# Optimization experiments

Hardware: AMD Instinct MI355X
Metric: run time of the kernel (lower is better)

## Reference

```python
import jax, jax.numpy as jnp
import numpy as np

NUM_WIRES = 14
LAYERS = 3
PPL = 3
BATCH = 1024
DIM = 2 ** NUM_WIRES


def setup_inputs() -> dict:
    key = jax.random.key(0)
    k1, k2, k3, k4, k5 = jax.random.split(key, 5)
    sr = jax.random.normal(k1, (BATCH, DIM), jnp.float32)
    si = jax.random.normal(k2, (BATCH, DIM), jnp.float32)
    norm = jnp.sqrt(jnp.sum(sr * sr + si * si, axis=1, keepdims=True))
    sr, si = sr / norm, si / norm  # normalized amplitude-encoded states
    weights = jax.random.normal(k3, (LAYERS, PPL, NUM_WIRES), jnp.float32)
    head_w = jax.random.normal(k4, (1, NUM_WIRES), jnp.float32) / np.sqrt(NUM_WIRES)
    head_b = jax.random.normal(k5, (1,), jnp.float32) * 0.01
    return {"state_real": sr, "state_imag": si, "weights": weights,
            "head_w": head_w, "head_b": head_b}


def _apply_ry_all(st, angles):
    # st: (B,)+(2,)*n complex; apply RY(angles[q]) on each wire q (RYs on distinct wires commute)
    half = angles * 0.5
    c, s = jnp.cos(half), jnp.sin(half)
    for q in range(NUM_WIRES):
        ax = 1 + q
        a0 = jnp.take(st, 0, axis=ax)
        a1 = jnp.take(st, 1, axis=ax)
        n0 = c[q] * a0 - s[q] * a1
        n1 = s[q] * a0 + c[q] * a1
        st = jnp.stack([n0, n1], axis=ax)
    return st


def _apply_cnot(st, ctrl, tgt):
    # flip target axis only where control bit == 1
    ctrl_ax, tgt_ax = 1 + ctrl, 1 + tgt
    flipped = jnp.flip(st, axis=tgt_ax)
    mask_shape = [1] * (NUM_WIRES + 1)
    mask_shape[ctrl_ax] = 2
    mask = (jnp.arange(2).reshape(mask_shape) == 1)
    return jnp.where(mask, flipped, st)


def _circuit(state, weights):
    # state: (B, DIM) complex64 -> PauliZ expvals (B, NUM_WIRES)
    st = state.reshape((-1,) + (2,) * NUM_WIRES)
    for l in range(LAYERS):
        # sequential RY(w[l,p,q]) for p=0..PPL-1 on wire q compose to RY(sum_p w[l,p,q])
        ang = jnp.sum(weights[l], axis=0)  # (NUM_WIRES,)
        st = _apply_ry_all(st, ang)
        for j in range(NUM_WIRES):
            st = _apply_cnot(st, j, (j + 1) % NUM_WIRES)
    probs = st.real ** 2 + st.imag ** 2  # (B,)+(2,)*n
    probs = probs.reshape(-1, DIM)
    idx = jnp.arange(DIM)
    # PennyLane convention: wire 0 is the most significant bit
    bits = (idx[None, :] >> (NUM_WIRES - 1 - jnp.arange(NUM_WIRES))[:, None]) & 1  # (n, DIM)
    signs = (1 - 2 * bits).astype(probs.dtype)
    return probs @ signs.T  # (B, n)


def reference(state_real, state_imag, weights, head_w, head_b):
    state = jax.lax.complex(state_real, state_imag)
    feats = _circuit(state, weights)  # (B, NUM_WIRES)
    return feats @ head_w[0] + head_b[0]  # (B,)
```

## Files before the change

kernel.cpp:

```cpp
#include <hip/hip_runtime.h>

typedef unsigned int u32;

#define DIM 16384
#define NT  512

__host__ __device__ constexpr u32 swzN(u32 d) {
    u32 b0 = ((d >> 4) ^ (d >> 5)) & 1u;
    u32 b1 = (d >> 4) & 1u;
    u32 b2 = ((d >> 7) ^ (d >> 8)) & 1u;
    u32 b3 = ((d >> 6) ^ (d >> 8)) & 1u;
    return d ^ b0 ^ (b1 << 1) ^ (b2 << 2) ^ (b3 << 3);
}

__host__ __device__ constexpr u32 mmap(u32 y) {
    u32 s = y;
    s ^= s >> 1; s ^= s >> 2; s ^= s >> 4; s ^= s >> 8;
    return (s & 0x1FFFu) | (((s ^ (y >> 13)) & 1u) << 13);
}

__host__ __device__ constexpr u32 mpow(u32 x, int L) {
    for (int i = 0; i < L; ++i) x = mmap(x);
    return x;
}

constexpr u32 PV3[5] = {0x040, 0x080, 0x100, 0x200, 0x400};
constexpr u32 PV4[5] = {0x006, 0x00C, 0x018, 0x030, 0x060};
constexpr u32 PV5[5] = {0x3001, 0x0003, 0x0C00, 0x1800, 0x3000};
constexpr u32 PV6[5] = {0x005, 0x00A, 0x014, 0x028, 0x050};
constexpr u32 PV7[5] = {0x0A0, 0x140, 0x280, 0x500, 0xA00};

__host__ __device__ constexpr u32 moff(const u32* v, int r) {
    u32 m = 0;
    for (int i = 0; i < 5; ++i) if ((r >> i) & 1) m ^= v[i];
    return m;
}
__host__ __device__ constexpr u32 parmask(const u32* v, int L, int b) {
    u32 pm = 0;
    for (int r = 0; r < 32; ++r)
        pm |= ((mpow(moff(v, r), L) >> b) & 1u) << r;
    return pm;
}
__host__ __device__ constexpr int hbit(int D) {
    int h = 0;
    while (D >> (h + 1)) ++h;
    return 1 << h;
}

__device__ __forceinline__ void rot2(float2& a0, float2& a1, float c, float s) {
    float t0x = s * a1.x, t0y = s * a1.y;
    float t1x = s * a0.x, t1y = s * a0.y;
    float n0x = fmaf(c, a0.x, -t0x), n0y = fmaf(c, a0.y, -t0y);
    float n1x = fmaf(c, a1.x,  t1x), n1y = fmaf(c, a1.y,  t1y);
    a0.x = n0x; a0.y = n0y;
    a1.x = n1x; a1.y = n1y;
}

template<int D, u32 PM>
__device__ __forceinline__ void gateGM(float2 (&am)[32], float c, float s, u32 sB) {
    constexpr int H = hbit(D);
    float sp = sB ? -s : s;
    #pragma unroll
    for (int r = 0; r < 32; ++r)
        if (!(r & H)) {
            if ((PM >> r) & 1) rot2(am[r], am[r ^ D], c, -sp);
            else               rot2(am[r], am[r ^ D], c,  sp);
        }
}

__global__ __launch_bounds__(NT, 2) void qsim_kernel(
    const float* __restrict__ sreal, const float* __restrict__ simag,
    const float* __restrict__ wts,   const float* __restrict__ hw,
    const float* __restrict__ hb,    float* __restrict__ out)
{
    extern __shared__ float smem[];
    float* angC   = smem + 32768;
    float* angS   = angC + 48;
    float* lutLo  = angS + 48;
    float* lutHi  = lutLo + 128;
    float* redbuf = lutHi + 128;
    float2* st2 = (float2*)smem;
    float4* stv = (float4*)smem;

    int tid = threadIdx.x;
    int b   = blockIdx.x;

    const float4* pr = (const float4*)(sreal + (size_t)b * DIM);
    const float4* pi = (const float4*)(simag + (size_t)b * DIM);
    float4 vr[8], vi[8];
    #pragma unroll
    for (int h = 0; h < 8; ++h) {
        vr[h] = pr[(h << 9) | tid];
        vi[h] = pi[(h << 9) | tid];
    }

    if (tid < 42) {
        int l = tid / 14, bb = tid % 14, q = 13 - bb;
        float a = 0.5f * (wts[l * 42 + q] + wts[l * 42 + 14 + q] + wts[l * 42 + 28 + q]);
        angC[l * 16 + bb] = cosf(a);
        angS[l * 16 + bb] = sinf(a);
    } else if (tid >= 64 && tid < 192) {
        int i = tid - 64;
        float ssum = 0.f;
        for (int bb = 0; bb < 7; ++bb) if ((i >> bb) & 1) ssum += hw[13 - bb];
        lutLo[i] = ssum;
    } else if (tid >= 192 && tid < 320) {
        int i = tid - 192;
        float ssum = 0.f;
        for (int bb = 0; bb < 7; ++bb) if ((i >> bb) & 1) ssum += hw[6 - bb];
        lutHi[i] = ssum;
    }

    float2 am[32];
    #pragma unroll
    for (int h = 0; h < 8; ++h) {
        am[h * 4 + 0] = make_float2(vr[h].x, vi[h].x);
        am[h * 4 + 1] = make_float2(vr[h].y, vi[h].y);
        am[h * 4 + 2] = make_float2(vr[h].z, vi[h].z);
        am[h * 4 + 3] = make_float2(vr[h].w, vi[h].w);
    }

    __syncthreads();
    float W0  = lutLo[127] + lutHi[127];
    float acc = 0.f;

    {
        gateGM< 1, 0>(am, angC[ 0], angS[ 0], 0);
        gateGM< 2, 0>(am, angC[ 1], angS[ 1], 0);
        gateGM< 4, 0>(am, angC[11], angS[11], 0);
        gateGM< 8, 0>(am, angC[12], angS[12], 0);
        gateGM<16, 0>(am, angC[13], angS[13], 0);
        u32 base = swzN((u32)tid << 2);
        bool sw = (((tid >> 2) ^ (tid >> 3)) & 1) != 0;
        #pragma unroll
        for (int h = 0; h < 8; ++h)
            #pragma unroll
            for (int m = 0; m < 2; ++m) {
                u32 idx = (base ^ swzN(((u32)h << 11) | ((u32)m << 1))) >> 1;
                int r = h * 4 + m * 2;
                float2 a0 = am[r], a1 = am[r + 1];
                stv[idx] = sw ? make_float4(a1.x, a1.y, a0.x, a0.y)
                              : make_float4(a0.x, a0.y, a1.x, a1.y);
            }
        __syncthreads();
    }

    {
        u32 yb = (((u32)tid & 1u) << 1) | (((u32)tid >> 1) << 6);
        u32 base = swzN(yb);
        #pragma unroll
        for (int h = 0; h < 16; ++h) {
            u32 idx = (base ^ swzN((u32)h << 2)) >> 1;
            float4 v = stv[idx];
            if (((h >> 2) ^ (h >> 3)) & 1) {
                am[h * 2 + 1] = make_float2(v.x, v.y);
                am[h * 2]     = make_float2(v.z, v.w);
            } else {
                am[h * 2]     = make_float2(v.x, v.y);
                am[h * 2 + 1] = make_float2(v.z, v.w);
            }
        }
        gateGM< 2, 0>(am, angC[2], angS[2], 0);
        gateGM< 4, 0>(am, angC[3], angS[3], 0);
        gateGM< 8, 0>(am, angC[4], angS[4], 0);
        gateGM<16, 0>(am, angC[5], angS[5], 0);
        #pragma unroll
        for (int h = 0; h < 16; ++h) {
            u32 idx = (base ^ swzN((u32)h << 2)) >> 1;
            float2 a0 = am[h * 2], a1 = am[h * 2 + 1];
            if (((h >> 2) ^ (h >> 3)) & 1) stv[idx] = make_float4(a1.x, a1.y, a0.x, a0.y);
            else                           stv[idx] = make_float4(a0.x, a0.y, a1.x, a1.y);
        }
        __syncthreads();
    }

    {
        u32 B = ((u32)tid & 63u) | (((u32)tid >> 6) << 11);
        u32 base = swzN(B);
        #pragma unroll
        for (int j = 0; j < 32; ++j) am[j] = st2[base ^ swzN((u32)j << 6)];
        gateGM< 1, 0>(am, angC[ 6], angS[ 6], 0);
        gateGM< 2, 0>(am, angC[ 7], angS[ 7], 0);
        gateGM< 4, 0>(am, angC[ 8], angS[ 8], 0);
        gateGM< 8, 0>(am, angC[ 9], angS[ 9], 0);
        gateGM<16, 0>(am, angC[10], angS[10], 0);
        u32 z1 = mmap(B);
        gateGM< 3, parmask(PV3, 1,  7)>(am, angC[16 +  7], angS[16 +  7], (z1 >>  7) & 1u);
        gateGM< 6, parmask(PV3, 1,  8)>(am, angC[16 +  8], angS[16 +  8], (z1 >>  8) & 1u);
        gateGM<12, parmask(PV3, 1,  9)>(am, angC[16 +  9], angS[16 +  9], (z1 >>  9) & 1u);
        gateGM<24, parmask(PV3, 1, 10)>(am, angC[16 + 10], angS[16 + 10], (z1 >> 10) & 1u);
        #pragma unroll
        for (int j = 0; j < 32; ++j) st2[base ^ swzN((u32)j << 6)] = am[j];
        __syncthreads();
    }

    {
        u32 B = ((u32)tid & 3u) | (((u32)tid >> 2) << 7);
        u32 base = swzN(B);
        #pragma unroll
        for (int r = 0; r < 32; ++r) am[r] = st2[base ^ swzN(moff(PV4, r))];
        u32 z1 = mmap(B);
        gateGM< 1, parmask(PV4, 1, 2)>(am, angC[16 + 2], angS[16 + 2], (z1 >> 2) & 1u);
        gateGM< 2, parmask(PV4, 1, 3)>(am, angC[16 + 3], angS[16 + 3], (z1 >> 3) & 1u);
        gateGM< 4, parmask(PV4, 1, 4)>(am, angC[16 + 4], angS[16 + 4], (z1 >> 4) & 1u);
        gateGM< 8, parmask(PV4, 1, 5)>(am, angC[16 + 5], angS[16 + 5], (z1 >> 5) & 1u);
        gateGM<16, parmask(PV4, 1, 6)>(am, angC[16 + 6], angS[16 + 6], (z1 >> 6) & 1u);
        #pragma unroll
        for (int r = 0; r < 32; ++r) st2[base ^ swzN(moff(PV4, r))] = am[r];
        __syncthreads();
    }

    {
        u32 B = (((u32)tid & 0xFFu) << 2) | (((u32)tid >> 8) << 13);
        u32 base = swzN(B);
        #pragma unroll
        for (int r = 0; r < 32; ++r) am[r] = st2[base ^ swzN(moff(PV5, r))];
        u32 z1 = mmap(B), z2 = mmap(z1);
        gateGM< 1, parmask(PV5, 1,  0)>(am, angC[16 +  0], angS[16 +  0], (z1 >>  0) & 1u);
        gateGM< 2, parmask(PV5, 1,  1)>(am, angC[16 +  1], angS[16 +  1], (z1 >>  1) & 1u);
        gateGM< 4, parmask(PV5, 1, 11)>(am, angC[16 + 11], angS[16 + 11], (z1 >> 11) & 1u);
        gateGM< 8, parmask(PV5, 1, 12)>(am, angC[16 + 12], angS[16 + 12], (z1 >> 12) & 1u);
        gateGM<16, parmask(PV5, 1, 13)>(am, angC[16 + 13], angS[16 + 13], (z1 >> 13) & 1u);
        gateGM<25, parmask(PV5, 2,  0)>(am, angC[32 +  0], angS[32 +  0], (z2 >>  0) & 1u);
        gateGM< 3, parmask(PV5, 2,  1)>(am, angC[32 +  1], angS[32 +  1], (z2 >>  1) & 1u);
        gateGM<12, parmask(PV5, 2, 12)>(am, angC[32 + 12], angS[32 + 12], (z2 >> 12) & 1u);
        gateGM<24, parmask(PV5, 2, 13)>(am, angC[32 + 13], angS[32 + 13], (z2 >> 13) & 1u);
        #pragma unroll
        for (int r = 0; r < 32; ++r) st2[base ^ swzN(moff(PV5, r))] = am[r];
        __syncthreads();
    }

    {
        u32 B = ((u32)tid & 3u) | (((u32)tid >> 2) << 7);
        u32 base = swzN(B);
        #pragma unroll
        for (int r = 0; r < 32; ++r) am[r] = st2[base ^ swzN(moff(PV6, r))];
        u32 z2 = mpow(B, 2);
        gateGM< 1, parmask(PV6, 2, 2)>(am, angC[32 + 2], angS[32 + 2], (z2 >> 2) & 1u);
        gateGM< 2, parmask(PV6, 2, 3)>(am, angC[32 + 3], angS[32 + 3], (z2 >> 3) & 1u);
        gateGM< 4, parmask(PV6, 2, 4)>(am, angC[32 + 4], angS[32 + 4], (z2 >> 4) & 1u);
        gateGM< 8, parmask(PV6, 2, 5)>(am, angC[32 + 5], angS[32 + 5], (z2 >> 5) & 1u);
        gateGM<16, parmask(PV6, 2, 6)>(am, angC[32 + 6], angS[32 + 6], (z2 >> 6) & 1u);
        #pragma unroll
        for (int r = 0; r < 32; ++r) st2[base ^ swzN(moff(PV6, r))] = am[r];
        __syncthreads();
    }

    {
        u32 B = ((u32)tid & 0x7Fu) | (((u32)tid >> 7) << 12);
        u32 base = swzN(B);
        #pragma unroll
        for (int r = 0; r < 32; ++r) am[r] = st2[base ^ swzN(moff(PV7, r))];
        u32 z2 = mpow(B, 2);
        gateGM< 1, parmask(PV7, 2,  7)>(am, angC[32 +  7], angS[32 +  7], (z2 >>  7) & 1u);
        gateGM< 2, parmask(PV7, 2,  8)>(am, angC[32 +  8], angS[32 +  8], (z2 >>  8) & 1u);
        gateGM< 4, parmask(PV7, 2,  9)>(am, angC[32 +  9], angS[32 +  9], (z2 >>  9) & 1u);
        gateGM< 8, parmask(PV7, 2, 10)>(am, angC[32 + 10], angS[32 + 10], (z2 >> 10) & 1u);
        gateGM<16, parmask(PV7, 2, 11)>(am, angC[32 + 11], angS[32 + 11], (z2 >> 11) & 1u);
        u32 wB = mmap(z2);
        #pragma unroll
        for (int r = 0; r < 32; ++r) {
            u32 w = wB ^ mpow(moff(PV7, r), 3);
            float p  = fmaf(am[r].x, am[r].x, am[r].y * am[r].y);
            float wv = W0 - 2.0f * (lutLo[w & 127u] + lutHi[w >> 7]);
            acc = fmaf(wv, p, acc);
        }
    }

    #pragma unroll
    for (int off = 32; off > 0; off >>= 1) acc += __shfl_xor(acc, off, 64);
    if ((tid & 63) == 0) redbuf[tid >> 6] = acc;
    __syncthreads();
    if (tid == 0) {
        float tot = hb[0];
        #pragma unroll
        for (int i = 0; i < 8; ++i) tot += redbuf[i];
        out[b] = tot;
    }
}

extern "C" void kernel_launch(void* const* d_in, const int* in_sizes, int n_in,
                              void* d_out, int out_size, void* d_ws, size_t ws_size,
                              hipStream_t stream)
{
    const float* sreal = (const float*)d_in[0];
    const float* simag = (const float*)d_in[1];
    const float* wts   = (const float*)d_in[2];
    const float* hw    = (const float*)d_in[3];
    const float* hb    = (const float*)d_in[4];
    float* out = (float*)d_out;

    int batch = in_sizes[0] / DIM;
    size_t smem_bytes = (32768 + 48 + 48 + 128 + 128 + 16) * sizeof(float);

    (void)hipFuncSetAttribute((const void*)qsim_kernel,
                              hipFuncAttributeMaxDynamicSharedMemorySize, (int)smem_bytes);
    qsim_kernel<<<dim3(batch), dim3(NT), smem_bytes, stream>>>(sreal, simag, wts, hw, hb, out);
}
```

Baseline: 208.9 us.

## Halve shared state buffer by exchanging in two half-block phases for occupancy

Each shared-memory transpose between gate groups is split into two rounds: half of the threads (selected by tid bit 6 or 7) write and read back their half of the state through a 64 KB buffer instead of 128 KB, using a compacted index. This halves LDS per block so launch bounds can request 4 blocks per SM instead of 2, aiming to improve latency hiding. It also drops the separate vr/vi staging registers. In exchange, each exchange now needs four barriers instead of one, and the higher occupancy target caps registers for the 32-element complex amplitude array, risking spills.

```diff
diff --git a/kernel.cpp b/kernel.cpp
--- a/kernel.cpp
+++ b/kernel.cpp
@@ -18,7 +18,6 @@
     s ^= s >> 1; s ^= s >> 2; s ^= s >> 4; s ^= s >> 8;
     return (s & 0x1FFFu) | (((s ^ (y >> 13)) & 1u) << 13);
 }
-
 __host__ __device__ constexpr u32 mpow(u32 x, int L) {
     for (int i = 0; i < L; ++i) x = mmap(x);
     return x;
@@ -45,6 +44,9 @@
     int h = 0;
     while (D >> (h + 1)) ++h;
     return 1 << h;
+}
+__host__ __device__ constexpr u32 cmpt(u32 s, int t) {
+    return (s & ((1u << t) - 1u)) | ((s >> (t + 1)) << t);
 }
 
 __device__ __forceinline__ void rot2(float2& a0, float2& a1, float c, float s) {
@@ -68,30 +70,216 @@
         }
 }
 
-__global__ __launch_bounds__(NT, 2) void qsim_kernel(
+__device__ __forceinline__ u32 B2of(int t) {
+    return ((u32)(t & 1) << 1) | ((u32)((t >> 1) & 3) << 6) | ((u32)((t >> 6) & 1) << 8)
+         | ((u32)((t >> 3) & 7) << 9) | ((u32)((t >> 7) & 3) << 12);
+}
+__device__ __forceinline__ u32 B3of(int t) { return ((u32)t & 63u) | (((u32)t >> 6) << 11); }
+__device__ __forceinline__ u32 B4of(int t) {
+    return (u32)(t & 3) | ((u32)((t >> 2) & 1) << 7) | ((u32)((t >> 6) & 1) << 8)
+         | ((u32)((t >> 3) & 7) << 9) | ((u32)((t >> 7) & 3) << 12);
+}
+__device__ __forceinline__ u32 B5of(int t) { return (((u32)t & 0xFFu) << 2) | (((u32)t >> 8) << 13); }
+__device__ __forceinline__ u32 B7of(int t) { return ((u32)t & 0x7Fu) | (((u32)t >> 7) << 12); }
+
+__device__ __forceinline__ void doG1(float2 (&am)[32], const float* angC, const float* angS) {
+    gateGM< 1, 0>(am, angC[ 0], angS[ 0], 0);
+    gateGM< 2, 0>(am, angC[ 1], angS[ 1], 0);
+    gateGM< 4, 0>(am, angC[11], angS[11], 0);
+    gateGM< 8, 0>(am, angC[12], angS[12], 0);
+    gateGM<16, 0>(am, angC[13], angS[13], 0);
+}
+__device__ __forceinline__ void doG2(float2 (&am)[32], const float* angC, const float* angS) {
+    gateGM< 2, 0>(am, angC[2], angS[2], 0);
+    gateGM< 4, 0>(am, angC[3], angS[3], 0);
+    gateGM< 8, 0>(am, angC[4], angS[4], 0);
+    gateGM<16, 0>(am, angC[5], angS[5], 0);
+}
+__device__ __forceinline__ void doG3(int tid, float2 (&am)[32], const float* angC, const float* angS) {
+    gateGM< 1, 0>(am, angC[ 6], angS[ 6], 0);
+    gateGM< 2, 0>(am, angC[ 7], angS[ 7], 0);
+    gateGM< 4, 0>(am, angC[ 8], angS[ 8], 0);
+    gateGM< 8, 0>(am, angC[ 9], angS[ 9], 0);
+    gateGM<16, 0>(am, angC[10], angS[10], 0);
+    u32 z1 = mmap(B3of(tid));
+    gateGM< 3, parmask(PV3, 1,  7)>(am, angC[16 +  7], angS[16 +  7], (z1 >>  7) & 1u);
+    gateGM< 6, parmask(PV3, 1,  8)>(am, angC[16 +  8], angS[16 +  8], (z1 >>  8) & 1u);
+    gateGM<12, parmask(PV3, 1,  9)>(am, angC[16 +  9], angS[16 +  9], (z1 >>  9) & 1u);
+    gateGM<24, parmask(PV3, 1, 10)>(am, angC[16 + 10], angS[16 + 10], (z1 >> 10) & 1u);
+}
+__device__ __forceinline__ void doG4(int tid, float2 (&am)[32], const float* angC, const float* angS) {
+    u32 z1 = mmap(B4of(tid));
+    gateGM< 1, parmask(PV4, 1, 2)>(am, angC[16 + 2], angS[16 + 2], (z1 >> 2) & 1u);
+    gateGM< 2, parmask(PV4, 1, 3)>(am, angC[16 + 3], angS[16 + 3], (z1 >> 3) & 1u);
+    gateGM< 4, parmask(PV4, 1, 4)>(am, angC[16 + 4], angS[16 + 4], (z1 >> 4) & 1u);
+    gateGM< 8, parmask(PV4, 1, 5)>(am, angC[16 + 5], angS[16 + 5], (z1 >> 5) & 1u);
+    gateGM<16, parmask(PV4, 1, 6)>(am, angC[16 + 6], angS[16 + 6], (z1 >> 6) & 1u);
+}
+__device__ __forceinline__ void doG5(int tid, float2 (&am)[32], const float* angC, const float* angS) {
+    u32 z1 = mmap(B5of(tid)), z2 = mmap(z1);
+    gateGM< 1, parmask(PV5, 1,  0)>(am, angC[16 +  0], angS[16 +  0], (z1 >>  0) & 1u);
+    gateGM< 2, parmask(PV5, 1,  1)>(am, angC[16 +  1], angS[16 +  1], (z1 >>  1) & 1u);
+    gateGM< 4, parmask(PV5, 1, 11)>(am, angC[16 + 11], angS[16 + 11], (z1 >> 11) & 1u);
+    gateGM< 8, parmask(PV5, 1, 12)>(am, angC[16 + 12], angS[16 + 12], (z1 >> 12) & 1u);
+    gateGM<16, parmask(PV5, 1, 13)>(am, angC[16 + 13], angS[16 + 13], (z1 >> 13) & 1u);
+    gateGM<25, parmask(PV5, 2,  0)>(am, angC[32 +  0], angS[32 +  0], (z2 >>  0) & 1u);
+    gateGM< 3, parmask(PV5, 2,  1)>(am, angC[32 +  1], angS[32 +  1], (z2 >>  1) & 1u);
+    gateGM<12, parmask(PV5, 2, 12)>(am, angC[32 + 12], angS[32 + 12], (z2 >> 12) & 1u);
+    gateGM<24, parmask(PV5, 2, 13)>(am, angC[32 + 13], angS[32 + 13], (z2 >> 13) & 1u);
+}
+__device__ __forceinline__ void doG6(int tid, float2 (&am)[32], const float* angC, const float* angS) {
+    u32 z2 = mpow(B4of(tid), 2);
+    gateGM< 1, parmask(PV6, 2, 2)>(am, angC[32 + 2], angS[32 + 2], (z2 >> 2) & 1u);
+    gateGM< 2, parmask(PV6, 2, 3)>(am, angC[32 + 3], angS[32 + 3], (z2 >> 3) & 1u);
+    gateGM< 4, parmask(PV6, 2, 4)>(am, angC[32 + 4], angS[32 + 4], (z2 >> 4) & 1u);
+    gateGM< 8, parmask(PV6, 2, 5)>(am, angC[32 + 5], angS[32 + 5], (z2 >> 5) & 1u);
+    gateGM<16, parmask(PV6, 2, 6)>(am, angC[32 + 6], angS[32 + 6], (z2 >> 6) & 1u);
+}
+__device__ __forceinline__ void doG7(int tid, float2 (&am)[32], const float* angC, const float* angS) {
+    u32 z2 = mpow(B7of(tid), 2);
+    gateGM< 1, parmask(PV7, 2,  7)>(am, angC[32 +  7], angS[32 +  7], (z2 >>  7) & 1u);
+    gateGM< 2, parmask(PV7, 2,  8)>(am, angC[32 +  8], angS[32 +  8], (z2 >>  8) & 1u);
+    gateGM< 4, parmask(PV7, 2,  9)>(am, angC[32 +  9], angS[32 +  9], (z2 >>  9) & 1u);
+    gateGM< 8, parmask(PV7, 2, 10)>(am, angC[32 + 10], angS[32 + 10], (z2 >> 10) & 1u);
+    gateGM<16, parmask(PV7, 2, 11)>(am, angC[32 + 11], angS[32 + 11], (z2 >> 11) & 1u);
+}
+__device__ __forceinline__ void doMeas(int tid, float2 (&am)[32], const float* lutLo,
+                                       const float* lutHi, float& acc, float W0) {
+    u32 wB = mpow(B7of(tid), 3);
+    #pragma unroll
+    for (int r = 0; r < 32; ++r) {
+        u32 w = wB ^ mpow(moff(PV7, r), 3);
+        float p  = fmaf(am[r].x, am[r].x, am[r].y * am[r].y);
+        float wv = W0 - 2.0f * (lutLo[w & 127u] + lutHi[w >> 7]);
+        acc = fmaf(wv, p, acc);
+    }
+}
+
+__device__ __forceinline__ void doW1(int tid, float* smem, float2 (&am)[32]) {
+    float4* stv = (float4*)smem;
+    u32 base = cmpt(swzN((u32)tid << 2), 8);
+    bool sw = (((tid >> 2) ^ (tid >> 3)) & 1) != 0;
+    #pragma unroll
+    for (int h = 0; h < 8; ++h)
+        #pragma unroll
+        for (int m = 0; m < 2; ++m) {
+            u32 idx = (base ^ (((u32)h << 10) | ((u32)m << 1))) >> 1;
+            int r = h * 4 + m * 2;
+            float2 a0 = am[r], a1 = am[r + 1];
+            stv[idx] = sw ? make_float4(a1.x, a1.y, a0.x, a0.y)
+                          : make_float4(a0.x, a0.y, a1.x, a1.y);
+        }
+}
+__device__ __forceinline__ void doR2(int tid, float* smem, float2 (&am)[32]) {
+    float4* stv = (float4*)smem;
+    u32 base = cmpt(swzN(B2of(tid)), 8);
+    #pragma unroll
+    for (int h = 0; h < 16; ++h) {
+        u32 idx = (base ^ swzN((u32)h << 2)) >> 1;
+        float4 v = stv[idx];
+        if (((h >> 2) ^ (h >> 3)) & 1) {
+            am[h * 2 + 1] = make_float2(v.x, v.y);
+            am[h * 2]     = make_float2(v.z, v.w);
+        } else {
+            am[h * 2]     = make_float2(v.x, v.y);
+            am[h * 2 + 1] = make_float2(v.z, v.w);
+        }
+    }
+}
+__device__ __forceinline__ void doW2(int tid, float* smem, float2 (&am)[32]) {
+    float4* stv = (float4*)smem;
+    u32 base = cmpt(swzN(B2of(tid)), 12);
+    #pragma unroll
+    for (int h = 0; h < 16; ++h) {
+        u32 idx = (base ^ swzN((u32)h << 2)) >> 1;
+        float2 a0 = am[h * 2], a1 = am[h * 2 + 1];
+        if (((h >> 2) ^ (h >> 3)) & 1) stv[idx] = make_float4(a1.x, a1.y, a0.x, a0.y);
+        else                           stv[idx] = make_float4(a0.x, a0.y, a1.x, a1.y);
+    }
+}
+__device__ __forceinline__ void doR3(int tid, float* smem, float2 (&am)[32]) {
+    float2* st2 = (float2*)smem;
+    u32 base = cmpt(swzN(B3of(tid)), 12);
+    #pragma unroll
+    for (int j = 0; j < 32; ++j) am[j] = st2[base ^ swzN((u32)j << 6)];
+}
+__device__ __forceinline__ void doW3(int tid, float* smem, float2 (&am)[32]) {
+    float2* st2 = (float2*)smem;
+    u32 base = cmpt(swzN(B3of(tid)), 12);
+    #pragma unroll
+    for (int j = 0; j < 32; ++j) st2[base ^ swzN((u32)j << 6)] = am[j];
+}
+__device__ __forceinline__ void doR4(int tid, float* smem, float2 (&am)[32]) {
+    float2* st2 = (float2*)smem;
+    u32 base = cmpt(swzN(B4of(tid)), 12);
+    #pragma unroll
+    for (int r = 0; r < 32; ++r) am[r] = st2[base ^ swzN(moff(PV4, r))];
+}
+__device__ __forceinline__ void doW4(int tid, float* smem, float2 (&am)[32]) {
+    float2* st2 = (float2*)smem;
+    u32 base = cmpt(swzN(B4of(tid)), 8);
+    #pragma unroll
+    for (int r = 0; r < 32; ++r) st2[base ^ swzN(moff(PV4, r))] = am[r];
+}
+__device__ __forceinline__ void doR5(int tid, float* smem, float2 (&am)[32]) {
+    float2* st2 = (float2*)smem;
+    u32 base = cmpt(swzN(B5of(tid)), 8);
+    #pragma unroll
+    for (int r = 0; r < 32; ++r) am[r] = st2[base ^ cmpt(moff(PV5, r), 8)];
+}
+__device__ __forceinline__ void doW5(int tid, float* smem, float2 (&am)[32]) {
+    float2* st2 = (float2*)smem;
+    u32 base = cmpt(swzN(B5of(tid)), 8);
+    #pragma unroll
+    for (int r = 0; r < 32; ++r) st2[base ^ cmpt(moff(PV5, r), 8)] = am[r];
+}
+__device__ __forceinline__ void doR6(int tid, float* smem, float2 (&am)[32]) {
+    float2* st2 = (float2*)smem;
+    u32 base = cmpt(swzN(B4of(tid)), 8);
+    #pragma unroll
+    for (int r = 0; r < 32; ++r) am[r] = st2[base ^ swzN(moff(PV6, r))];
+}
+__device__ __forceinline__ void doW6(int tid, float* smem, float2 (&am)[32]) {
+    float2* st2 = (float2*)smem;
+    u32 base = cmpt(swzN(B4of(tid)), 12);
+    #pragma unroll
+    for (int r = 0; r < 32; ++r) st2[base ^ swzN(moff(PV6, r))] = am[r];
+}
+__device__ __forceinline__ void doR7(int tid, float* smem, float2 (&am)[32]) {
+    float2* st2 = (float2*)smem;
+    u32 base = cmpt(swzN(B7of(tid)), 12);
+    #pragma unroll
+    for (int r = 0; r < 32; ++r) am[r] = st2[base ^ swzN(moff(PV7, r))];
+}
+
+__global__ __launch_bounds__(NT, 4) void qsim_kernel(
     const float* __restrict__ sreal, const float* __restrict__ simag,
     const float* __restrict__ wts,   const float* __restrict__ hw,
     const float* __restrict__ hb,    float* __restrict__ out)
 {
     extern __shared__ float smem[];
-    float* angC   = smem + 32768;
+    float* angC   = smem + 16384;
     float* angS   = angC + 48;
     float* lutLo  = angS + 48;
     float* lutHi  = lutLo + 128;
     float* redbuf = lutHi + 128;
-    float2* st2 = (float2*)smem;
-    float4* stv = (float4*)smem;
 
     int tid = threadIdx.x;
     int b   = blockIdx.x;
+    int r6  = (tid >> 6) & 1;
+    int r7  = (tid >> 7) & 1;
 
     const float4* pr = (const float4*)(sreal + (size_t)b * DIM);
     const float4* pi = (const float4*)(simag + (size_t)b * DIM);
-    float4 vr[8], vi[8];
+    float2 am[32];
     #pragma unroll
     for (int h = 0; h < 8; ++h) {
-        vr[h] = pr[(h << 9) | tid];
-        vi[h] = pi[(h << 9) | tid];
+        float4 r = pr[(h << 9) | tid];
+        float4 i = pi[(h << 9) | tid];
+        am[h * 4 + 0] = make_float2(r.x, i.x);
+        am[h * 4 + 1] = make_float2(r.y, i.y);
+        am[h * 4 + 2] = make_float2(r.z, i.z);
+        am[h * 4 + 3] = make_float2(r.w, i.w);
     }
 
     if (tid < 42) {
@@ -111,161 +299,42 @@
         lutHi[i] = ssum;
     }
 
-    float2 am[32];
-    #pragma unroll
-    for (int h = 0; h < 8; ++h) {
-        am[h * 4 + 0] = make_float2(vr[h].x, vi[h].x);
-        am[h * 4 + 1] = make_float2(vr[h].y, vi[h].y);
-        am[h * 4 + 2] = make_float2(vr[h].z, vi[h].z);
-        am[h * 4 + 3] = make_float2(vr[h].w, vi[h].w);
-    }
-
     __syncthreads();
     float W0  = lutLo[127] + lutHi[127];
     float acc = 0.f;
 
-    {
-        gateGM< 1, 0>(am, angC[ 0], angS[ 0], 0);
-        gateGM< 2, 0>(am, angC[ 1], angS[ 1], 0);
-        gateGM< 4, 0>(am, angC[11], angS[11], 0);
-        gateGM< 8, 0>(am, angC[12], angS[12], 0);
-        gateGM<16, 0>(am, angC[13], angS[13], 0);
-        u32 base = swzN((u32)tid << 2);
-        bool sw = (((tid >> 2) ^ (tid >> 3)) & 1) != 0;
-        #pragma unroll
-        for (int h = 0; h < 8; ++h)
-            #pragma unroll
-            for (int m = 0; m < 2; ++m) {
-                u32 idx = (base ^ swzN(((u32)h << 11) | ((u32)m << 1))) >> 1;
-                int r = h * 4 + m * 2;
-                float2 a0 = am[r], a1 = am[r + 1];
-                stv[idx] = sw ? make_float4(a1.x, a1.y, a0.x, a0.y)
-                              : make_float4(a0.x, a0.y, a1.x, a1.y);
-            }
-        __syncthreads();
-    }
-
-    {
-        u32 yb = (((u32)tid & 1u) << 1) | (((u32)tid >> 1) << 6);
-        u32 base = swzN(yb);
-        #pragma unroll
-        for (int h = 0; h < 16; ++h) {
-            u32 idx = (base ^ swzN((u32)h << 2)) >> 1;
-            float4 v = stv[idx];
-            if (((h >> 2) ^ (h >> 3)) & 1) {
-                am[h * 2 + 1] = make_float2(v.x, v.y);
-                am[h * 2]     = make_float2(v.z, v.w);
-            } else {
-                am[h * 2]     = make_float2(v.x, v.y);
-                am[h * 2 + 1] = make_float2(v.z, v.w);
-            }
-        }
-        gateGM< 2, 0>(am, angC[2], angS[2], 0);
-        gateGM< 4, 0>(am, angC[3], angS[3], 0);
-        gateGM< 8, 0>(am, angC[4], angS[4], 0);
-        gateGM<16, 0>(am, angC[5], angS[5], 0);
-        #pragma unroll
-        for (int h = 0; h < 16; ++h) {
-            u32 idx = (base ^ swzN((u32)h << 2)) >> 1;
-            float2 a0 = am[h * 2], a1 = am[h * 2 + 1];
-            if (((h >> 2) ^ (h >> 3)) & 1) stv[idx] = make_float4(a1.x, a1.y, a0.x, a0.y);
-            else                           stv[idx] = make_float4(a0.x, a0.y, a1.x, a1.y);
-        }
-        __syncthreads();
-    }
-
-    {
-        u32 B = ((u32)tid & 63u) | (((u32)tid >> 6) << 11);
-        u32 base = swzN(B);
-        #pragma unroll
-        for (int j = 0; j < 32; ++j) am[j] = st2[base ^ swzN((u32)j << 6)];
-        gateGM< 1, 0>(am, angC[ 6], angS[ 6], 0);
-        gateGM< 2, 0>(am, angC[ 7], angS[ 7], 0);
-        gateGM< 4, 0>(am, angC[ 8], angS[ 8], 0);
-        gateGM< 8, 0>(am, angC[ 9], angS[ 9], 0);
-        gateGM<16, 0>(am, angC[10], angS[10], 0);
-        u32 z1 = mmap(B);
-        gateGM< 3, parmask(PV3, 1,  7)>(am, angC[16 +  7], angS[16 +  7], (z1 >>  7) & 1u);
-        gateGM< 6, parmask(PV3, 1,  8)>(am, angC[16 +  8], angS[16 +  8], (z1 >>  8) & 1u);
-        gateGM<12, parmask(PV3, 1,  9)>(am, angC[16 +  9], angS[16 +  9], (z1 >>  9) & 1u);
-        gateGM<24, parmask(PV3, 1, 10)>(am, angC[16 + 10], angS[16 + 10], (z1 >> 10) & 1u);
-        #pragma unroll
-        for (int j = 0; j < 32; ++j) st2[base ^ swzN((u32)j << 6)] = am[j];
-        __syncthreads();
-    }
-
-    {
-        u32 B = ((u32)tid & 3u) | (((u32)tid >> 2) << 7);
-        u32 base = swzN(B);
-        #pragma unroll
-        for (int r = 0; r < 32; ++r) am[r] = st2[base ^ swzN(moff(PV4, r))];
-        u32 z1 = mmap(B);
-        gateGM< 1, parmask(PV4, 1, 2)>(am, angC[16 + 2], angS[16 + 2], (z1 >> 2) & 1u);
-        gateGM< 2, parmask(PV4, 1, 3)>(am, angC[16 + 3], angS[16 + 3], (z1 >> 3) & 1u);
-        gateGM< 4, parmask(PV4, 1, 4)>(am, angC[16 + 4], angS[16 + 4], (z1 >> 4) & 1u);
-        gateGM< 8, parmask(PV4, 1, 5)>(am, angC[16 + 5], angS[16 + 5], (z1 >> 5) & 1u);
-        gateGM<16, parmask(PV4, 1, 6)>(am, angC[16 + 6], angS[16 + 6], (z1 >> 6) & 1u);
-        #pragma unroll
-        for (int r = 0; r < 32; ++r) st2[base ^ swzN(moff(PV4, r))] = am[r];
-        __syncthreads();
-    }
-
-    {
-        u32 B = (((u32)tid & 0xFFu) << 2) | (((u32)tid >> 8) << 13);
-        u32 base = swzN(B);
-        #pragma unroll
-        for (int r = 0; r < 32; ++r) am[r] = st2[base ^ swzN(moff(PV5, r))];
-        u32 z1 = mmap(B), z2 = mmap(z1);
-        gateGM< 1, parmask(PV5, 1,  0)>(am, angC[16 +  0], angS[16 +  0], (z1 >>  0) & 1u);
-        gateGM< 2, parmask(PV5, 1,  1)>(am, angC[16 +  1], angS[16 +  1], (z1 >>  1) & 1u);
-        gateGM< 4, parmask(PV5, 1, 11)>(am, angC[16 + 11], angS[16 + 11], (z1 >> 11) & 1u);
-        gateGM< 8, parmask(PV5, 1, 12)>(am, angC[16 + 12], angS[16 + 12], (z1 >> 12) & 1u);
-        gateGM<16, parmask(PV5, 1, 13)>(am, angC[16 + 13], angS[16 + 13], (z1 >> 13) & 1u);
-        gateGM<25, parmask(PV5, 2,  0)>(am, angC[32 +  0], angS[32 +  0], (z2 >>  0) & 1u);
-        gateGM< 3, parmask(PV5, 2,  1)>(am, angC[32 +  1], angS[32 +  1], (z2 >>  1) & 1u);
-        gateGM<12, parmask(PV5, 2, 12)>(am, angC[32 + 12], angS[32 + 12], (z2 >> 12) & 1u);
-        gateGM<24, parmask(PV5, 2, 13)>(am, angC[32 + 13], angS[32 + 13], (z2 >> 13) & 1u);
-        #pragma unroll
-        for (int r = 0; r < 32; ++r) st2[base ^ swzN(moff(PV5, r))] = am[r];
-        __syncthreads();
-    }
-
-    {
-        u32 B = ((u32)tid & 3u) | (((u32)tid >> 2) << 7);
-        u32 base = swzN(B);
-        #pragma unroll
-        for (int r = 0; r < 32; ++r) am[r] = st2[base ^ swzN(moff(PV6, r))];
-        u32 z2 = mpow(B, 2);
-        gateGM< 1, parmask(PV6, 2, 2)>(am, angC[32 + 2], angS[32 + 2], (z2 >> 2) & 1u);
-        gateGM< 2, parmask(PV6, 2, 3)>(am, angC[32 + 3], angS[32 + 3], (z2 >> 3) & 1u);
-        gateGM< 4, parmask(PV6, 2, 4)>(am, angC[32 + 4], angS[32 + 4], (z2 >> 4) & 1u);
-        gateGM< 8, parmask(PV6, 2, 5)>(am, angC[32 + 5], angS[32 + 5], (z2 >> 5) & 1u);
-        gateGM<16, parmask(PV6, 2, 6)>(am, angC[32 + 6], angS[32 + 6], (z2 >> 6) & 1u);
-        #pragma unroll
-        for (int r = 0; r < 32; ++r) st2[base ^ swzN(moff(PV6, r))] = am[r];
-        __syncthreads();
-    }
-
-    {
-        u32 B = ((u32)tid & 0x7Fu) | (((u32)tid >> 7) << 12);
-        u32 base = swzN(B);
-        #pragma unroll
-        for (int r = 0; r < 32; ++r) am[r] = st2[base ^ swzN(moff(PV7, r))];
-        u32 z2 = mpow(B, 2);
-        gateGM< 1, parmask(PV7, 2,  7)>(am, angC[32 +  7], angS[32 +  7], (z2 >>  7) & 1u);
-        gateGM< 2, parmask(PV7, 2,  8)>(am, angC[32 +  8], angS[32 +  8], (z2 >>  8) & 1u);
-        gateGM< 4, parmask(PV7, 2,  9)>(am, angC[32 +  9], angS[32 +  9], (z2 >>  9) & 1u);
-        gateGM< 8, parmask(PV7, 2, 10)>(am, angC[32 + 10], angS[32 + 10], (z2 >> 10) & 1u);
-        gateGM<16, parmask(PV7, 2, 11)>(am, angC[32 + 11], angS[32 + 11], (z2 >> 11) & 1u);
-        u32 wB = mmap(z2);
-        #pragma unroll
-        for (int r = 0; r < 32; ++r) {
-            u32 w = wB ^ mpow(moff(PV7, r), 3);
-            float p  = fmaf(am[r].x, am[r].x, am[r].y * am[r].y);
-            float wv = W0 - 2.0f * (lutLo[w & 127u] + lutHi[w >> 7]);
-            acc = fmaf(wv, p, acc);
-        }
-    }
+    doG1(am, angC, angS);
+    if (r6 == 0) doW1(tid, smem, am);  __syncthreads();
+    if (r6 == 0) doR2(tid, smem, am);  __syncthreads();
+    if (r6 == 1) doW1(tid, smem, am);  __syncthreads();
+    if (r6 == 1) doR2(tid, smem, am);  __syncthreads();
+    doG2(am, angC, angS);
+    if (r7 == 0) doW2(tid, smem, am);  __syncthreads();
+    if (r7 == 0) doR3(tid, smem, am);  __syncthreads();
+    if (r7 == 1) doW2(tid, smem, am);  __syncthreads();
+    if (r7 == 1) doR3(tid, smem, am);  __syncthreads();
+    doG3(tid, am, angC, angS);
+    if (r7 == 0) doW3(tid, smem, am);  __syncthreads();
+    if (r7 == 0) doR4(tid, smem, am);  __syncthreads();
+    if (r7 == 1) doW3(tid, smem, am);  __syncthreads();
+    if (r7 == 1) doR4(tid, smem, am);  __syncthreads();
+    doG4(tid, am, angC, angS);
+    if (r6 == 0) doW4(tid, smem, am);  __syncthreads();
+    if (r6 == 0) doR5(tid, smem, am);  __syncthreads();
+    if (r6 == 1) doW4(tid, smem, am);  __syncthreads();
+    if (r6 == 1) doR5(tid, smem, am);  __syncthreads();
+    doG5(tid, am, angC, angS);
+    if (r6 == 0) doW5(tid, smem, am);  __syncthreads();
+    if (r6 == 0) doR6(tid, smem, am);  __syncthreads();
+    if (r6 == 1) doW5(tid, smem, am);  __syncthreads();
+    if (r6 == 1) doR6(tid, smem, am);  __syncthreads();
+    doG6(tid, am, angC, angS);
+    if (r7 == 0) doW6(tid, smem, am);  __syncthreads();
+    if (r7 == 0) doR7(tid, smem, am);  __syncthreads();
+    if (r7 == 1) doW6(tid, smem, am);  __syncthreads();
+    if (r7 == 1) doR7(tid, smem, am);  __syncthreads();
+    doG7(tid, am, angC, angS);
+    doMeas(tid, am, lutLo, lutHi, acc, W0);
 
     #pragma unroll
     for (int off = 32; off > 0; off >>= 1) acc += __shfl_xor(acc, off, 64);
@@ -291,7 +360,7 @@
     float* out = (float*)d_out;
 
     int batch = in_sizes[0] / DIM;
-    size_t smem_bytes = (32768 + 48 + 48 + 128 + 128 + 16) * sizeof(float);
+    size_t smem_bytes = (16384 + 48 + 48 + 128 + 128 + 8) * sizeof(float);
 
     (void)hipFuncSetAttribute((const void*)qsim_kernel,
                               hipFuncAttributeMaxDynamicSharedMemorySize, (int)smem_bytes);
```

Result: slower. 250.8 us (+20.0%).
